# Performance work log

Measured on AMD Instinct MI355X. Metric: run time of the kernel, lower is better.

Reference implementation:

```python
import jax, jax.numpy as jnp
import numpy as np

# Standard FP4 E2M1 lookup table (nvfp4-style): sign bit in nibble MSB.
FP4_LUT = jnp.array([0.0, 0.5, 1.0, 1.5, 2.0, 3.0, 4.0, 6.0,
                     -0.0, -0.5, -1.0, -1.5, -2.0, -3.0, -4.0, -6.0],
                    dtype=jnp.float32)


def dequant_fp4(packed_i32, scales, group_size):
    """packed_i32: [K/8, N] int32 (8 fp4 nibbles per word, low nibble first);
    scales: [K/group_size, N]. Returns dense fp32 weight [K, N]."""
    w = jax.lax.bitcast_convert_type(packed_i32, jnp.uint32)  # [K/8, N]
    # Unpack nibbles along the reduction axis: nibble i -> row 8*r + i.
    nib = jnp.stack([(w >> jnp.uint32(4 * i)) & jnp.uint32(0xF) for i in range(8)],
                    axis=1)                                    # [K/8, 8, N]
    K = nib.shape[0] * 8
    nib = nib.reshape(K, w.shape[1])                           # [K, N]
    vals = FP4_LUT[nib]                                        # [K, N]
    s = jnp.repeat(scales, group_size, axis=0)                 # [K, N]
    return vals * s


def setup_inputs() -> dict:
    key = jax.random.key(0)
    k1, k2, k3, k4, k5, k6 = jax.random.split(key, 6)
    tokens, H, I, G = 4096, 2048, 5632, 128
    return {
        "hidden": jax.random.normal(k1, (tokens, H), dtype=jnp.float32),
        "moe_output": jax.random.normal(k2, (tokens, H), dtype=jnp.float32),
        "gate_up_weights": jax.random.randint(k3, (H // 8, 2 * I), 0, 2147483647, dtype=jnp.int32),
        "gate_up_scales": jax.random.uniform(k4, (H // G, 2 * I), dtype=jnp.float32, minval=0.01, maxval=0.1),
        "down_weights": jax.random.randint(k5, (I // 8, H), 0, 2147483647, dtype=jnp.int32),
        "down_scales": jax.random.uniform(k6, (I // G, H), dtype=jnp.float32, minval=0.01, maxval=0.1),
        "group_size": G,
    }


def reference(hidden, moe_output, gate_up_weights, gate_up_scales,
              down_weights, down_scales, group_size):
    # Shared-expert SwiGLU FFN with FP4 group-quantized weights, fused residual add.
    W_gu = dequant_fp4(gate_up_weights, gate_up_scales, group_size)  # [H, 2I]
    gu = hidden @ W_gu                                               # [T, 2I]
    I = gu.shape[1] // 2
    gate, up = gu[:, :I], gu[:, I:]
    act = jax.nn.silu(gate) * up                                     # [T, I]
    W_d = dequant_fp4(down_weights, down_scales, group_size)         # [I, H]
    return moe_output + act @ W_d                                    # [T, H]
```

## Files before the change

### kernel.cpp

```cpp
#include <hip/hip_runtime.h>
#include <hip/hip_fp16.h>
#include <stdint.h>

#define TOKENS 4096
#define HDIM   2048
#define IDIM   5632
#define BM 128
#define BN 128
#define BK 64

#define G1_NP  11264
#define G1_KSB (G1_NP * 64)

typedef _Float16 f16x8 __attribute__((ext_vector_type(8)));
typedef float    f32x4 __attribute__((ext_vector_type(4)));

__device__ __forceinline__ uint32_t dec2(uint32_t z, uint32_t s2u) {
    uint32_t sgn = (z << 12) & 0x80008000u;
    uint32_t h   = ((z << 9) & 0x0E000E00u) | sgn;
    __half2 hv = __builtin_bit_cast(__half2, h);
    __half2 sv = __builtin_bit_cast(__half2, s2u);
    __half2 r  = __hmul2(hv, sv);
    return __builtin_bit_cast(uint32_t, r);
}
__device__ __forceinline__ int4 dec8(uint32_t w, uint32_t s2u) {
    int4 d;
    d.x = (int)dec2( w        & 0x000F000Fu, s2u);
    d.y = (int)dec2((w >> 4)  & 0x000F000Fu, s2u);
    d.z = (int)dec2((w >> 8)  & 0x000F000Fu, s2u);
    d.w = (int)dec2((w >> 12) & 0x000F000Fu, s2u);
    return d;
}
__device__ __forceinline__ uint32_t scale_s2u(float sc) {
    uint16_t hs = __builtin_bit_cast(uint16_t, __float2half(sc * 16384.0f));
    return (uint32_t)hs * 0x00010001u;
}
__device__ __forceinline__ uint32_t packh(float lo, float hi) {
    __half2 h2 = __halves2half2(__float2half(lo), __float2half(hi));
    return __builtin_bit_cast(uint32_t, h2);
}
__device__ __forceinline__ void gl_lds16(const void* g, void* l) {
    __builtin_amdgcn_global_load_lds(
        (const __attribute__((address_space(1))) uint32_t*)g,
        (__attribute__((address_space(3))) uint32_t*)l, 16, 0, 0);
}

__global__ __launch_bounds__(256) void convert_hidden(
    const float* __restrict__ src, __half* __restrict__ dst)
{
    int idx = blockIdx.x * 256 + threadIdx.x;
    const float4* s = (const float4*)src + (size_t)idx * 2;
    float4 a = s[0], b = s[1];
    int4 v;
    v.x = (int)packh(a.x, b.x);
    v.y = (int)packh(a.y, b.y);
    v.z = (int)packh(a.z, b.z);
    v.w = (int)packh(a.w, b.w);
    *((int4*)dst + idx) = v;
}

__global__ __launch_bounds__(256) void dequant_wgu5(
    const uint32_t* __restrict__ W, const float* __restrict__ S,
    __half* __restrict__ Bt)
{
    __shared__ __half L[256 * 64];
    const int kt = blockIdx.y;
    const int t  = threadIdx.x;
    const int np = blockIdx.x * 256 + t;
    const int sc = (np >> 6) * 32 + (np & 31) + (((np >> 5) & 1) ? IDIM : 0);
    uint32_t s2u = scale_s2u(S[(size_t)(kt >> 1) * (2 * IDIM) + sc]);
    #pragma unroll
    for (int j = 0; j < 8; ++j) {
        uint32_t w = W[(size_t)(kt * 8 + j) * (2 * IDIM) + sc];
        int4 d = dec8(w, s2u);
        *(int4*)&L[t * 64 + ((j ^ (t & 7)) << 3)] = d;
    }
    __syncthreads();
    __half* dst = Bt + (size_t)kt * G1_KSB + (size_t)blockIdx.x * 256 * 64;
    #pragma unroll
    for (int k = 0; k < 8; ++k) {
        int c = k * 256 + t;
        int row = c >> 3, s = c & 7;
        int4 d = *(const int4*)&L[row * 64 + ((s ^ (row & 7)) << 3)];
        *(int4*)(dst + c * 8) = d;
    }
}

__global__ __launch_bounds__(256, 4) void gemm1_s(
    const __half* __restrict__ A, const __half* __restrict__ Bt,
    __half* __restrict__ act)
{
    __shared__ __half Alds[BM * 64];
    __shared__ __half Blds[BN * 64];
    const int tid  = threadIdx.x;
    const int lane = tid & 63;
    const int wid  = tid >> 6;
    const int wm = wid >> 1, wn = wid & 1;
    const int m0 = blockIdx.y * BM;
    const int n0 = blockIdx.x * BN;

    f32x4 acc[4][4];
    #pragma unroll
    for (int i = 0; i < 4; ++i)
        #pragma unroll
        for (int j = 0; j < 4; ++j) acc[i][j] = f32x4{0.f, 0.f, 0.f, 0.f};

    const __half* srcA[4];
    const __half* srcB[4];
    #pragma unroll
    for (int i = 0; i < 4; ++i) {
        int u = i * 256 + tid, row = u >> 3, s = u & 7, sl = s ^ (row & 7);
        srcA[i] = A  + (size_t)(m0 + row) * HDIM + sl * 8;
        srcB[i] = Bt + (size_t)(n0 + row) * 64 + sl * 8;
    }

    int aoff[4][2], boff[4][2];
    #pragma unroll
    for (int f = 0; f < 4; ++f)
        #pragma unroll
        for (int ks = 0; ks < 2; ++ks) {
            int kb = ks * 4 + (lane >> 4);
            int ra = wm * 64 + f * 16 + (lane & 15);
            int rb = wn * 64 + f * 16 + (lane & 15);
            aoff[f][ks] = ra * 128 + ((kb ^ (ra & 7)) << 4);
            boff[f][ks] = rb * 128 + ((kb ^ (rb & 7)) << 4);
        }

    for (int kt = 0; kt < HDIM / 64; ++kt) {
        #pragma unroll
        for (int i = 0; i < 4; ++i) {
            int u = i * 256 + tid;
            gl_lds16(srcA[i], (char*)Alds + u * 16);
            gl_lds16(srcB[i], (char*)Blds + u * 16);
            srcA[i] += 64;
            srcB[i] += G1_KSB;
        }
        __syncthreads();
        #pragma unroll
        for (int ks = 0; ks < 2; ++ks) {
            f16x8 af[4], bf[4];
            #pragma unroll
            for (int f = 0; f < 4; ++f) {
                af[f] = *(const f16x8*)((const char*)Alds + aoff[f][ks]);
                bf[f] = *(const f16x8*)((const char*)Blds + boff[f][ks]);
            }
            #pragma unroll
            for (int mi = 0; mi < 4; ++mi)
                #pragma unroll
                for (int ni = 0; ni < 4; ++ni)
                    acc[mi][ni] = __builtin_amdgcn_mfma_f32_16x16x32_f16(af[mi], bf[ni], acc[mi][ni], 0, 0, 0);
        }
        __syncthreads();
    }

    const int pairbase = ((n0 + wn * 64) >> 6) * 32;
    #pragma unroll
    for (int mi = 0; mi < 4; ++mi) {
        #pragma unroll
        for (int q = 0; q < 2; ++q) {
            int gcol = pairbase + q * 16 + (lane & 15);
            int colstore = (gcol & ~7) | (((gcol & 3) << 1) | ((gcol >> 2) & 1));
            #pragma unroll
            for (int r = 0; r < 4; ++r) {
                int m = m0 + wm * 64 + mi * 16 + (lane >> 4) * 4 + r;
                float gv = acc[mi][q][r];
                float uv = acc[mi][q + 2][r];
                float sig = 1.0f / (1.0f + __expf(-gv));
                act[(size_t)m * IDIM + colstore] = __float2half(gv * sig * uv);
            }
        }
    }
}

__global__ __launch_bounds__(256, 2) void gemm1_silu(
    const __half* __restrict__ A, const uint32_t* __restrict__ W,
    const float* __restrict__ S, __half* __restrict__ act)
{
    __shared__ __half Alds[BM * BK];
    __shared__ __half Blds[2][BN * BK];
    const int tid  = threadIdx.x;
    const int lane = tid & 63;
    const int wid  = tid >> 6;
    const int wm = wid >> 1, wn = wid & 1;
    const int m0 = blockIdx.y * BM;
    const int c0 = blockIdx.x * BN;

    f32x4 accg[4][4], accu[4][4];
    #pragma unroll
    for (int i = 0; i < 4; ++i)
        #pragma unroll
        for (int j = 0; j < 4; ++j) {
            accg[i][j] = f32x4{0.f, 0.f, 0.f, 0.f};
            accu[i][j] = f32x4{0.f, 0.f, 0.f, 0.f};
        }

    const int c = tid & 127;
    const int rbase = (tid >> 7) * 4;

    for (int kt = 0; kt < HDIM / BK; ++kt) {
        const int k0 = kt * BK;
        #pragma unroll
        for (int i = 0; i < 4; ++i) {
            int u = tid + i * 256;
            int row = u >> 3, kb = u & 7;
            int4 v = *(const int4*)(A + (size_t)(m0 + row) * HDIM + k0 + kb * 8);
            *(int4*)((char*)Alds + row * 128 + ((kb ^ (row & 7)) << 4)) = v;
        }
        const int g = k0 >> 7;
        #pragma unroll
        for (int p = 0; p < 2; ++p) {
            const int ncol = (p ? IDIM : 0) + c0 + c;
            uint32_t s2u = scale_s2u(S[(size_t)g * (2 * IDIM) + ncol]);
            #pragma unroll
            for (int i = 0; i < 4; ++i) {
                int rl = rbase + i;
                uint32_t w = W[(size_t)(kt * 8 + rl) * (2 * IDIM) + ncol];
                int4 d = dec8(w, s2u);
                *(int4*)((char*)&Blds[p][0] + c * 128 + ((rl ^ (c & 7)) << 4)) = d;
            }
        }
        __syncthreads();
        #pragma unroll
        for (int ks = 0; ks < 2; ++ks) {
            f16x8 af[4], bg[4], bu[4];
            const int kb = ks * 4 + (lane >> 4);
            #pragma unroll
            for (int mi = 0; mi < 4; ++mi) {
                int m = wm * 64 + mi * 16 + (lane & 15);
                af[mi] = *(const f16x8*)((const char*)Alds + m * 128 + ((kb ^ (m & 7)) << 4));
            }
            #pragma unroll
            for (int ni = 0; ni < 4; ++ni) {
                int n = wn * 64 + ni * 16 + (lane & 15);
                bg[ni] = *(const f16x8*)((const char*)&Blds[0][0] + n * 128 + ((kb ^ (n & 7)) << 4));
                bu[ni] = *(const f16x8*)((const char*)&Blds[1][0] + n * 128 + ((kb ^ (n & 7)) << 4));
            }
            #pragma unroll
            for (int mi = 0; mi < 4; ++mi)
                #pragma unroll
                for (int ni = 0; ni < 4; ++ni) {
                    accg[mi][ni] = __builtin_amdgcn_mfma_f32_16x16x32_f16(af[mi], bg[ni], accg[mi][ni], 0, 0, 0);
                    accu[mi][ni] = __builtin_amdgcn_mfma_f32_16x16x32_f16(af[mi], bu[ni], accu[mi][ni], 0, 0, 0);
                }
        }
        __syncthreads();
    }
    #pragma unroll
    for (int mi = 0; mi < 4; ++mi) {
        #pragma unroll
        for (int ni = 0; ni < 4; ++ni) {
            int nlog = c0 + wn * 64 + ni * 16 + (lane & 15);
            int ncol = (nlog & ~7) | (((nlog & 3) << 1) | ((nlog >> 2) & 1));
            #pragma unroll
            for (int r = 0; r < 4; ++r) {
                int m = m0 + wm * 64 + mi * 16 + (lane >> 4) * 4 + r;
                float gv = accg[mi][ni][r];
                float uv = accu[mi][ni][r];
                float sig = 1.0f / (1.0f + __expf(-gv));
                act[(size_t)m * IDIM + ncol] = __float2half(gv * sig * uv);
            }
        }
    }
}

__global__ __launch_bounds__(256, 2) void gemm2_add(
    const __half* __restrict__ A, const uint32_t* __restrict__ W,
    const float* __restrict__ S, const float* __restrict__ moe,
    float* __restrict__ out)
{
    __shared__ __half Alds[BM * BK];
    __shared__ __half Blds[BN * BK];
    const int tid  = threadIdx.x;
    const int lane = tid & 63;
    const int wid  = tid >> 6;
    const int wm = wid >> 1, wn = wid & 1;
    const int m0 = blockIdx.y * BM;
    const int n0 = blockIdx.x * BN;

    f32x4 acc[4][4];
    #pragma unroll
    for (int i = 0; i < 4; ++i)
        #pragma unroll
        for (int j = 0; j < 4; ++j) acc[i][j] = f32x4{0.f, 0.f, 0.f, 0.f};

    const int c = tid & 127;
    const int rbase = (tid >> 7) * 4;

    int aoff[4][2], boff[4][2];
    #pragma unroll
    for (int f = 0; f < 4; ++f)
        #pragma unroll
        for (int ks = 0; ks < 2; ++ks) {
            int kb = ks * 4 + (lane >> 4);
            int ra = wm * 64 + f * 16 + (lane & 15);
            int rb = wn * 64 + f * 16 + (lane & 15);
            aoff[f][ks] = ra * 128 + ((kb ^ (ra & 7)) << 4);
            boff[f][ks] = rb * 128 + ((kb ^ (rb & 7)) << 4);
        }

    for (int kt = 0; kt < IDIM / BK; ++kt) {
        const int k0 = kt * BK;
        #pragma unroll
        for (int i = 0; i < 4; ++i) {
            int u = tid + i * 256;
            int row = u >> 3, kb = u & 7;
            int4 v = *(const int4*)(A + (size_t)(m0 + row) * IDIM + k0 + kb * 8);
            *(int4*)((char*)Alds + row * 128 + ((kb ^ (row & 7)) << 4)) = v;
        }
        {
            const int g = k0 >> 7;
            const int ncol = n0 + c;
            uint32_t s2u = scale_s2u(S[(size_t)g * HDIM + ncol]);
            #pragma unroll
            for (int i = 0; i < 4; ++i) {
                int rl = rbase + i;
                uint32_t w = W[(size_t)(kt * 8 + rl) * HDIM + ncol];
                int4 d = dec8(w, s2u);
                *(int4*)((char*)Blds + c * 128 + ((rl ^ (c & 7)) << 4)) = d;
            }
        }
        __syncthreads();
        #pragma unroll
        for (int ks = 0; ks < 2; ++ks) {
            f16x8 af[4], bf[4];
            #pragma unroll
            for (int f = 0; f < 4; ++f) {
                af[f] = *(const f16x8*)((const char*)Alds + aoff[f][ks]);
                bf[f] = *(const f16x8*)((const char*)Blds + boff[f][ks]);
            }
            #pragma unroll
            for (int mi = 0; mi < 4; ++mi)
                #pragma unroll
                for (int ni = 0; ni < 4; ++ni)
                    acc[mi][ni] = __builtin_amdgcn_mfma_f32_16x16x32_f16(af[mi], bf[ni], acc[mi][ni], 0, 0, 0);
        }
        __syncthreads();
    }
    #pragma unroll
    for (int mi = 0; mi < 4; ++mi) {
        #pragma unroll
        for (int ni = 0; ni < 4; ++ni) {
            int n = n0 + wn * 64 + ni * 16 + (lane & 15);
            #pragma unroll
            for (int r = 0; r < 4; ++r) {
                int m = m0 + wm * 64 + mi * 16 + (lane >> 4) * 4 + r;
                out[(size_t)m * HDIM + n] = moe[(size_t)m * HDIM + n] + acc[mi][ni][r];
            }
        }
    }
}

extern "C" void kernel_launch(void* const* d_in, const int* in_sizes, int n_in,
                              void* d_out, int out_size, void* d_ws, size_t ws_size,
                              hipStream_t stream) {
    const float*    hidden = (const float*)d_in[0];
    const float*    moe    = (const float*)d_in[1];
    const uint32_t* wgu    = (const uint32_t*)d_in[2];
    const float*    sgu    = (const float*)d_in[3];
    const uint32_t* wd     = (const uint32_t*)d_in[4];
    const float*    sd     = (const float*)d_in[5];
    float* out = (float*)d_out;

    const size_t sz_hidden = (size_t)TOKENS * HDIM * 2;
    const size_t sz_act    = (size_t)TOKENS * IDIM * 2;
    const size_t sz_wgu16  = (size_t)HDIM * 2 * IDIM * 2;

    __half* hidden_f16 = (__half*)d_ws;
    __half* act        = (__half*)((char*)d_ws + sz_hidden);
    __half* wgu16      = (__half*)((char*)d_ws + sz_hidden + sz_act);

    const size_t need_g1 = sz_hidden + sz_act + sz_wgu16;

    convert_hidden<<<dim3(TOKENS * HDIM / 8 / 256), dim3(256), 0, stream>>>(hidden, hidden_f16);

    if (ws_size >= need_g1) {
        dequant_wgu5<<<dim3(G1_NP / 256, 32), dim3(256), 0, stream>>>(wgu, sgu, wgu16);
        gemm1_s<<<dim3(G1_NP / BN, TOKENS / BM), dim3(256), 0, stream>>>(hidden_f16, wgu16, act);
    } else {
        gemm1_silu<<<dim3(IDIM / BN, TOKENS / BM), dim3(256), 0, stream>>>(hidden_f16, wgu, sgu, act);
    }

    gemm2_add<<<dim3(HDIM / BN, TOKENS / BM), dim3(256), 0, stream>>>(act, wd, sd, moe, out);
}
```

Measured before the change: 324.3 us.

## Pre-dequantize down weights into tiled fp16 workspace for second GEMM

Adds a separate dequant kernel that expands the FP4 down-projection weights into K-tiled fp16 layout in workspace, plus a new gemm2_s that streams A and B straight into LDS with direct loads and runs MFMA without decoding inside the loop. This mirrors the path already used for gemm1. It removes per-tile FP4 decode work from the GEMM inner loop, at the cost of an extra kernel launch and about 23 MB of fp16 weight write and read traffic. The new path runs only when the workspace is large enough.

```diff
diff --git a/kernel.cpp b/kernel.cpp
--- a/kernel.cpp
+++ b/kernel.cpp
@@ -11,6 +11,7 @@
 
 #define G1_NP  11264
 #define G1_KSB (G1_NP * 64)
+#define G2_KSB (HDIM * 64)
 
 typedef _Float16 f16x8 __attribute__((ext_vector_type(8)));
 typedef float    f32x4 __attribute__((ext_vector_type(4)));
@@ -86,6 +87,32 @@
     }
 }
 
+__global__ __launch_bounds__(256) void dequant_wd5(
+    const uint32_t* __restrict__ W, const float* __restrict__ S,
+    __half* __restrict__ Bt)
+{
+    __shared__ __half L[256 * 64];
+    const int kt = blockIdx.y;
+    const int t  = threadIdx.x;
+    const int n  = blockIdx.x * 256 + t;
+    uint32_t s2u = scale_s2u(S[(size_t)(kt >> 1) * HDIM + n]);
+    #pragma unroll
+    for (int j = 0; j < 8; ++j) {
+        uint32_t w = W[(size_t)(kt * 8 + j) * HDIM + n];
+        int4 d = dec8(w, s2u);
+        *(int4*)&L[t * 64 + ((j ^ (t & 7)) << 3)] = d;
+    }
+    __syncthreads();
+    __half* dst = Bt + (size_t)kt * G2_KSB + (size_t)blockIdx.x * 256 * 64;
+    #pragma unroll
+    for (int k = 0; k < 8; ++k) {
+        int c = k * 256 + t;
+        int row = c >> 3, s = c & 7;
+        int4 d = *(const int4*)&L[row * 64 + ((s ^ (row & 7)) << 3)];
+        *(int4*)(dst + c * 8) = d;
+    }
+}
+
 __global__ __launch_bounds__(256, 4) void gemm1_s(
     const __half* __restrict__ A, const __half* __restrict__ Bt,
     __half* __restrict__ act)
@@ -167,6 +194,86 @@
                 float uv = acc[mi][q + 2][r];
                 float sig = 1.0f / (1.0f + __expf(-gv));
                 act[(size_t)m * IDIM + colstore] = __float2half(gv * sig * uv);
+            }
+        }
+    }
+}
+
+__global__ __launch_bounds__(256, 4) void gemm2_s(
+    const __half* __restrict__ A, const __half* __restrict__ Bt,
+    const float* __restrict__ moe, float* __restrict__ out)
+{
+    __shared__ __half Alds[BM * 64];
+    __shared__ __half Blds[BN * 64];
+    const int tid  = threadIdx.x;
+    const int lane = tid & 63;
+    const int wid  = tid >> 6;
+    const int wm = wid >> 1, wn = wid & 1;
+    const int m0 = blockIdx.y * BM;
+    const int n0 = blockIdx.x * BN;
+
+    f32x4 acc[4][4];
+    #pragma unroll
+    for (int i = 0; i < 4; ++i)
+        #pragma unroll
+        for (int j = 0; j < 4; ++j) acc[i][j] = f32x4{0.f, 0.f, 0.f, 0.f};
+
+    const __half* srcA[4];
+    const __half* srcB[4];
+    #pragma unroll
+    for (int i = 0; i < 4; ++i) {
+        int u = i * 256 + tid, row = u >> 3, s = u & 7, sl = s ^ (row & 7);
+        srcA[i] = A  + (size_t)(m0 + row) * IDIM + sl * 8;
+        srcB[i] = Bt + (size_t)(n0 + row) * 64 + sl * 8;
+    }
+
+    int aoff[4][2], boff[4][2];
+    #pragma unroll
+    for (int f = 0; f < 4; ++f)
+        #pragma unroll
+        for (int ks = 0; ks < 2; ++ks) {
+            int kb = ks * 4 + (lane >> 4);
+            int ra = wm * 64 + f * 16 + (lane & 15);
+            int rb = wn * 64 + f * 16 + (lane & 15);
+            aoff[f][ks] = ra * 128 + ((kb ^ (ra & 7)) << 4);
+            boff[f][ks] = rb * 128 + ((kb ^ (rb & 7)) << 4);
+        }
+
+    for (int kt = 0; kt < IDIM / 64; ++kt) {
+        #pragma unroll
+        for (int i = 0; i < 4; ++i) {
+            int u = i * 256 + tid;
+            gl_lds16(srcA[i], (char*)Alds + u * 16);
+            gl_lds16(srcB[i], (char*)Blds + u * 16);
+            srcA[i] += 64;
+            srcB[i] += G2_KSB;
+        }
+        __syncthreads();
+        #pragma unroll
+        for (int ks = 0; ks < 2; ++ks) {
+            f16x8 af[4], bf[4];
+            #pragma unroll
+            for (int f = 0; f < 4; ++f) {
+                af[f] = *(const f16x8*)((const char*)Alds + aoff[f][ks]);
+                bf[f] = *(const f16x8*)((const char*)Blds + boff[f][ks]);
+            }
+            #pragma unroll
+            for (int mi = 0; mi < 4; ++mi)
+                #pragma unroll
+                for (int ni = 0; ni < 4; ++ni)
+                    acc[mi][ni] = __builtin_amdgcn_mfma_f32_16x16x32_f16(af[mi], bf[ni], acc[mi][ni], 0, 0, 0);
+        }
+        __syncthreads();
+    }
+    #pragma unroll
+    for (int mi = 0; mi < 4; ++mi) {
+        #pragma unroll
+        for (int ni = 0; ni < 4; ++ni) {
+            int n = n0 + wn * 64 + ni * 16 + (lane & 15);
+            #pragma unroll
+            for (int r = 0; r < 4; ++r) {
+                int m = m0 + wm * 64 + mi * 16 + (lane >> 4) * 4 + r;
+                out[(size_t)m * HDIM + n] = moe[(size_t)m * HDIM + n] + acc[mi][ni][r];
             }
         }
     }
@@ -364,12 +471,15 @@
     const size_t sz_hidden = (size_t)TOKENS * HDIM * 2;
     const size_t sz_act    = (size_t)TOKENS * IDIM * 2;
     const size_t sz_wgu16  = (size_t)HDIM * 2 * IDIM * 2;
+    const size_t sz_wd16   = (size_t)IDIM * HDIM * 2;
 
     __half* hidden_f16 = (__half*)d_ws;
     __half* act        = (__half*)((char*)d_ws + sz_hidden);
     __half* wgu16      = (__half*)((char*)d_ws + sz_hidden + sz_act);
+    __half* wd16       = (__half*)((char*)d_ws + sz_hidden + sz_act + sz_wgu16);
 
     const size_t need_g1 = sz_hidden + sz_act + sz_wgu16;
+    const size_t need_g2 = need_g1 + sz_wd16;
 
     convert_hidden<<<dim3(TOKENS * HDIM / 8 / 256), dim3(256), 0, stream>>>(hidden, hidden_f16);
 
@@ -380,5 +490,10 @@
         gemm1_silu<<<dim3(IDIM / BN, TOKENS / BM), dim3(256), 0, stream>>>(hidden_f16, wgu, sgu, act);
     }
 
-    gemm2_add<<<dim3(HDIM / BN, TOKENS / BM), dim3(256), 0, stream>>>(act, wd, sd, moe, out);
-}
+    if (ws_size >= need_g2) {
+        dequant_wd5<<<dim3(HDIM / 256, IDIM / 64), dim3(256), 0, stream>>>(wd, sd, wd16);
+        gemm2_s<<<dim3(HDIM / BN, TOKENS / BM), dim3(256), 0, stream>>>(act, wd16, moe, out);
+    } else {
+        gemm2_add<<<dim3(HDIM / BN, TOKENS / BM), dim3(256), 0, stream>>>(act, wd, sd, moe, out);
+    }
+}
```

Result: faster. 317.7 us (-2.0%).
